# Performance work log

Measured on AMD Instinct MI355X. Metric: run time of the kernel, lower is better.

## Reference

```python
import jax, jax.numpy as jnp
import numpy as np

B, S, H, T, W = 8, 512, 768, 4, 10
NEG = -1e9

def _u(key, shape, k):
    return jax.random.uniform(key, shape, jnp.float32, -k, k)

def setup_inputs():
    key = jax.random.key(0)
    ks = jax.random.split(key, 20)
    kh = float(1.0 / np.sqrt(H)); kt = float(1.0 / np.sqrt(T))
    return dict(
        embeddings=jax.random.normal(ks[0], (B, S, H), jnp.float32),
        l1f_wih=_u(ks[1], (4 * H, H), kh), l1f_whh=_u(ks[2], (4 * H, H), kh), l1f_b=_u(ks[3], (4 * H,), kh),
        l1r_wih=_u(ks[4], (4 * H, H), kh), l1r_whh=_u(ks[5], (4 * H, H), kh), l1r_b=_u(ks[6], (4 * H,), kh),
        attn_w=_u(ks[7], (3 * H,), kh), attn_b=_u(ks[8], (1,), kh),
        l2f_wih=_u(ks[9], (4 * T, 2 * H), kt), l2f_whh=_u(ks[10], (4 * T, T), kt), l2f_b=_u(ks[11], (4 * T,), kt),
        l2r_wih=_u(ks[12], (4 * T, 2 * H), kt), l2r_whh=_u(ks[13], (4 * T, T), kt), l2r_b=_u(ks[14], (4 * T,), kt),
        crf_start=0.1 * jax.random.normal(ks[15], (T,), jnp.float32),
        crf_end=0.1 * jax.random.normal(ks[16], (T,), jnp.float32),
        crf_trans=0.1 * jax.random.normal(ks[17], (T, T), jnp.float32),
        window_size=W,
    )

def _lstm_dir(x, w_ih, w_hh, b):
    # x: [B,S,D] -> [B,S,Hh]; torch gate order i,f,g,o
    Hh = w_hh.shape[1]
    bs = x.shape[0]
    xs = (jnp.einsum('bsd,gd->bsg', x, w_ih) + b).transpose(1, 0, 2)  # [S,B,4Hh]
    def step(carry, xt):
        h, c = carry
        g = xt + h @ w_hh.T
        i, f, gg, o = jnp.split(g, 4, axis=-1)
        c = jax.nn.sigmoid(f) * c + jax.nn.sigmoid(i) * jnp.tanh(gg)
        h = jax.nn.sigmoid(o) * jnp.tanh(c)
        return (h, c), h
    init = (jnp.zeros((bs, Hh), x.dtype), jnp.zeros((bs, Hh), x.dtype))
    _, hs = jax.lax.scan(step, init, xs)
    return hs.transpose(1, 0, 2)

def _bilstm(x, pf, pr):
    hf = _lstm_dir(x, *pf)
    hr = _lstm_dir(x[:, ::-1], *pr)[:, ::-1]
    return jnp.concatenate([hf, hr], axis=-1)

def _win_attn(h, w, b, win):
    # h: [B,S,D]; similarity(hi,hj) = w1.hi + w2.hj + w3.(hi*hj) + b
    bs, s, d = h.shape
    w1, w2, w3 = w[:d], w[d:2 * d], w[2 * d:]
    offs = jnp.arange(-win, win + 1)                      # [K]
    idx = jnp.arange(s)[:, None] + offs[None, :]          # [S,K]
    valid = (idx >= 0) & (idx < s)
    idxc = jnp.clip(idx, 0, s - 1)
    hw = h[:, idxc]                                       # [B,S,K,D]
    scores = (h @ w1)[:, :, None] \
        + jnp.einsum('bskd,d->bsk', hw, w2) \
        + jnp.einsum('bsd,bskd->bsk', h * w3, hw) + b[0]
    scores = jnp.where(valid[None], scores, NEG)
    aw = jax.nn.softmax(scores, axis=-1)                  # [B,S,K]
    return jnp.einsum('bsk,bskd->bsd', aw, hw)

def _viterbi(em, start, end, trans):
    # em: [B,S,T] -> tags [B,S]
    score0 = start[None] + em[:, 0]
    ems = em.transpose(1, 0, 2)[1:]                       # [S-1,B,T]
    def step(score, e_t):
        nxt = score[:, :, None] + trans[None]             # [B,Tprev,T]
        best = jnp.max(nxt, axis=1) + e_t
        bp = jnp.argmax(nxt, axis=1)
        return best, bp
    final, bps = jax.lax.scan(step, score0, ems)          # bps [S-1,B,T]
    final = final + end[None]
    last = jnp.argmax(final, axis=-1)                     # [B]
    def back(tag, bp):
        prev = jnp.take_along_axis(bp, tag[:, None], axis=1)[:, 0]
        return prev, prev
    _, tags_rev = jax.lax.scan(back, last, bps[::-1])
    return jnp.concatenate([tags_rev[::-1], last[None]], axis=0).transpose(1, 0)

def reference(embeddings, l1f_wih, l1f_whh, l1f_b, l1r_wih, l1r_whh, l1r_b,
              attn_w, attn_b, l2f_wih, l2f_whh, l2f_b, l2r_wih, l2r_whh, l2r_b,
              crf_start, crf_end, crf_trans, window_size):
    h1 = _bilstm(embeddings, (l1f_wih, l1f_whh, l1f_b), (l1r_wih, l1r_whh, l1r_b))
    d = h1.shape[-1] // 2
    hs = h1[..., :d] + h1[..., d:]                        # sum of directions [B,S,H]
    att = _win_attn(hs, attn_w, attn_b, int(window_size))
    x2 = jnp.concatenate([hs, att], axis=-1)              # [B,S,2H]
    h2 = _bilstm(x2, (l2f_wih, l2f_whh, l2f_b), (l2r_wih, l2r_whh, l2r_b))
    d2 = h2.shape[-1] // 2
    em = h2[..., :d2] + h2[..., d2:]                      # CRF emissions [B,S,T]
    tags = _viterbi(em, crf_start, crf_end, crf_trans)
    return tags, em
```

## Files before the change

kernel.cpp:

```cpp
#include <hip/hip_runtime.h>
#include <math.h>

#define SEQ 512
#define BATCH 8
#define HID 768
#define G4 3072
#define CHUNK 128
#define NEGV (-1000000000.0f)

typedef float v4f __attribute__((ext_vector_type(4)));

__device__ __forceinline__ float sigm(float x) { return 1.0f / (1.0f + expf(-x)); }

__device__ __forceinline__ float wred(float x) {
#pragma unroll
  for (int off = 32; off > 0; off >>= 1) x += __shfl_xor(x, off, 64);
  return x;
}

__device__ __forceinline__ void load2_f4_sc(const float* p0, const float* p1,
                                            v4f& a, v4f& b) {
  asm volatile("global_load_dwordx4 %0, %2, off sc0 sc1\n\t"
               "global_load_dwordx4 %1, %3, off sc0 sc1\n\t"
               "s_waitcnt vmcnt(0)"
               : "=&v"(a), "=&v"(b) : "v"(p0), "v"(p1) : "memory");
}
__device__ __forceinline__ int load_i_sc(const int* p) {
  int r;
  asm volatile("global_load_dword %0, %1, off sc0 sc1\n\ts_waitcnt vmcnt(0)"
               : "=v"(r) : "v"(p) : "memory");
  return r;
}
__device__ __forceinline__ void store_f_sc(float* p, float v) {
  asm volatile("global_store_dword %0, %1, off sc0 sc1" :: "v"(p), "v"(v) : "memory");
}
__device__ __forceinline__ void store_i_sc(int* p, int v) {
  asm volatile("global_store_dword %0, %1, off sc0 sc1" :: "v"(p), "v"(v) : "memory");
}

template <int CTRL, int RMASK>
__device__ __forceinline__ float dpp_add(float x) {
  int y = __builtin_amdgcn_update_dpp(0, __float_as_int(x), CTRL, RMASK, 0xF, false);
  return x + __int_as_float(y);
}
__device__ __forceinline__ float reduce32(float x) {
  x = dpp_add<0x121, 0xF>(x);
  x = dpp_add<0x122, 0xF>(x);
  x = dpp_add<0x124, 0xF>(x);
  x = dpp_add<0x128, 0xF>(x);
  x = dpp_add<0x142, 0xA>(x);
  return x;
}

__global__ void k_init(float* __restrict__ hbuf, int* __restrict__ flags) {
  int i = blockIdx.x * blockDim.x + threadIdx.x;
  if (i < 2 * 2 * BATCH * HID) hbuf[i] = 0.0f;
  if (i < 4096) flags[i] = 0;
}

__global__ __launch_bounds__(256) void k_proj1(
    const float* __restrict__ emb,
    const float* __restrict__ w_f, const float* __restrict__ b_f,
    const float* __restrict__ w_r, const float* __restrict__ b_r,
    float* __restrict__ xs_f, float* __restrict__ xs_r, int chunk) {
  __shared__ float As[16][132];
  __shared__ float Bs[16][132];
  const int tid = threadIdx.x;
  const int bn0 = blockIdx.x * 128;
  const int bb  = blockIdx.y;
  const int dir = blockIdx.z;
  const float* W    = dir ? w_r : w_f;
  const float* bias = dir ? b_r : b_f;
  float* xs = dir ? xs_r : xs_f;

  float acc[8][8];
#pragma unroll
  for (int i = 0; i < 8; i++)
#pragma unroll
    for (int j = 0; j < 8; j++) acc[i][j] = 0.0f;

  const int mload = tid & 127;
  const int kq0   = tid >> 7;
  const int tglob = dir ? (SEQ - 1 - (chunk * CHUNK + mload)) : (chunk * CHUNK + mload);
  const float* arow = emb + (size_t)(bb * SEQ + tglob) * HID;
  const float* brow = W + (size_t)(bn0 + mload) * HID;
  const int tm = tid & 15, tn = tid >> 4;

  for (int kt = 0; kt < HID; kt += 16) {
#pragma unroll
    for (int rep = 0; rep < 2; rep++) {
      int kq = kq0 + rep * 2;
      float4 a = *(const float4*)(arow + kt + kq * 4);
      As[kq * 4 + 0][mload] = a.x; As[kq * 4 + 1][mload] = a.y;
      As[kq * 4 + 2][mload] = a.z; As[kq * 4 + 3][mload] = a.w;
      float4 b = *(const float4*)(brow + kt + kq * 4);
      Bs[kq * 4 + 0][mload] = b.x; Bs[kq * 4 + 1][mload] = b.y;
      Bs[kq * 4 + 2][mload] = b.z; Bs[kq * 4 + 3][mload] = b.w;
    }
    __syncthreads();
#pragma unroll
    for (int k = 0; k < 16; k++) {
      float4 a0 = *(const float4*)&As[k][tm * 8];
      float4 a1 = *(const float4*)&As[k][tm * 8 + 4];
      float4 b0 = *(const float4*)&Bs[k][tn * 8];
      float4 b1 = *(const float4*)&Bs[k][tn * 8 + 4];
      float av[8] = {a0.x, a0.y, a0.z, a0.w, a1.x, a1.y, a1.z, a1.w};
      float bv[8] = {b0.x, b0.y, b0.z, b0.w, b1.x, b1.y, b1.z, b1.w};
#pragma unroll
      for (int i = 0; i < 8; i++)
#pragma unroll
        for (int j = 0; j < 8; j++) acc[i][j] += av[i] * bv[j];
    }
    __syncthreads();
  }
#pragma unroll
  for (int i = 0; i < 8; i++) {
    int row = tm * 8 + i;
    size_t base = (size_t)(bb * CHUNK + row) * G4 + bn0 + tn * 8;
#pragma unroll
    for (int j = 0; j < 8; j++) xs[base + j] = acc[i][j] + bias[bn0 + tn * 8 + j];
  }
}

__global__ __launch_bounds__(384, 2) void k_rec1(
    const float* __restrict__ whh_f, const float* __restrict__ whh_r,
    const float* __restrict__ xs_f, const float* __restrict__ xs_r,
    float* __restrict__ hbuf, float* __restrict__ cbuf, int* __restrict__ flags,
    float* __restrict__ hf, float* __restrict__ hr, int t0, int init) {
  __shared__ float hlds[4 * HID];
  const int tid = threadIdx.x;
  const int bid = blockIdx.x;
  const int dir = bid >> 7;
  const int bh  = (bid >> 6) & 1;
  const int jb  = bid & 63;
  const int J0  = jb * 12;
  const int grp = dir * 2 + bh;
  const int g  = tid >> 5;
  const int kq = tid & 31;
  const int j  = J0 + g;

  const float* W  = dir ? whh_r : whh_f;
  const float* xs = dir ? xs_r  : xs_f;
  float* harr = dir ? hr : hf;

  float wreg[4][24];
#pragma unroll
  for (int gate = 0; gate < 4; gate++) {
#pragma unroll
    for (int q = 0; q < 6; q++) {
      *(v4f*)&wreg[gate][q * 4] =
          *(const v4f*)&W[(size_t)(gate * HID + j) * HID + q * 128 + kq * 4];
    }
  }

  float cc[4];
#pragma unroll
  for (int b = 0; b < 4; b++) cc[b] = 0.0f;
  if (!init && kq == 16) {
#pragma unroll
    for (int b = 0; b < 4; b++) cc[b] = cbuf[bid * 48 + g * 4 + b];
  }

  for (int stp = 0; stp < CHUNK; stp++) {
    const int s = t0 + stp;
    const int par = s & 1;

    float xsv[4][4];
    if (kq == 16) {
#pragma unroll
      for (int b = 0; b < 4; b++) {
        const size_t xbase = (size_t)((bh * 4 + b) * CHUNK + stp) * G4 + j;
#pragma unroll
        for (int gate = 0; gate < 4; gate++)
          xsv[b][gate] = xs[xbase + gate * HID];
      }
    }

    if (tid < 64) {
      const int* fp = flags + (grp * 64 + tid) * 16;
      while (load_i_sc(fp) < s) { __builtin_amdgcn_s_sleep(4); }
    }
    __syncthreads();

    {
      const float* src = hbuf + (size_t)((par * 2 + dir) * BATCH + bh * 4) * HID + tid * 8;
      v4f a, b4;
      load2_f4_sc(src, src + 4, a, b4);
      *(v4f*)&hlds[tid * 8]     = a;
      *(v4f*)&hlds[tid * 8 + 4] = b4;
    }
    __syncthreads();

    float acc[4][4];
#pragma unroll
    for (int gate = 0; gate < 4; gate++)
#pragma unroll
      for (int b = 0; b < 4; b++) acc[gate][b] = 0.0f;
#pragma unroll
    for (int b = 0; b < 4; b++) {
      float hk[24];
#pragma unroll
      for (int q = 0; q < 6; q++)
        *(v4f*)&hk[q * 4] = *(const v4f*)&hlds[b * HID + q * 128 + kq * 4];
#pragma unroll
      for (int gate = 0; gate < 4; gate++)
#pragma unroll
        for (int k = 0; k < 24; k++) acc[gate][b] += wreg[gate][k] * hk[k];
    }
#pragma unroll
    for (int gate = 0; gate < 4; gate++)
#pragma unroll
      for (int b = 0; b < 4; b++) acc[gate][b] = reduce32(acc[gate][b]);

    if (kq == 16) {
      const int t = dir ? (SEQ - 1 - s) : s;
#pragma unroll
      for (int b = 0; b < 4; b++) {
        const int bg = bh * 4 + b;
        float iv = acc[0][b] + xsv[b][0];
        float fv = acc[1][b] + xsv[b][1];
        float gv = acc[2][b] + xsv[b][2];
        float ov = acc[3][b] + xsv[b][3];
        cc[b] = sigm(fv) * cc[b] + sigm(iv) * tanhf(gv);
        float h = sigm(ov) * tanhf(cc[b]);
        store_f_sc(hbuf + (size_t)(((par ^ 1) * 2 + dir) * BATCH + bg) * HID + j, h);
        harr[(size_t)(bg * SEQ + t) * HID + j] = h;
      }
    }
    asm volatile("s_waitcnt vmcnt(0)" ::: "memory");
    __syncthreads();
    if (tid == 0) store_i_sc(flags + (grp * 64 + jb) * 16, s + 1);
  }
  if (kq == 16) {
#pragma unroll
    for (int b = 0; b < 4; b++) cbuf[bid * 48 + g * 4 + b] = cc[b];
  }
}

__global__ void k_sum(float* __restrict__ hf, const float* __restrict__ hr) {
  int i = blockIdx.x * 256 + threadIdx.x;
  float4 a = ((const float4*)hf)[i];
  float4 b = ((const float4*)hr)[i];
  a.x += b.x; a.y += b.y; a.z += b.z; a.w += b.w;
  ((float4*)hf)[i] = a;
}

__global__ __launch_bounds__(64) void k_attn(
    const float* __restrict__ hs, const float* __restrict__ attn_w,
    const float* __restrict__ attn_b, float* __restrict__ att) {
  const int l = threadIdx.x;
  const int s = blockIdx.x, b = blockIdx.y;
  const float* hrow = hs + (size_t)(b * SEQ + s) * HID;
  float v[12];
  float u1p = 0.0f;
#pragma unroll
  for (int jj = 0; jj < 12; jj++) {
    int d = l + 64 * jj;
    float x = hrow[d];
    u1p += x * attn_w[d];
    v[jj] = attn_w[HID + d] + x * attn_w[2 * HID + d];
  }
  float u1 = wred(u1p) + attn_b[0];
  float sc[21];
  for (int o = 0; o < 21; o++) {
    int s2 = s + o - 10;
    if (s2 >= 0 && s2 < SEQ) {
      const float* h2 = hs + (size_t)(b * SEQ + s2) * HID;
      float p = 0.0f;
#pragma unroll
      for (int jj = 0; jj < 12; jj++) p += h2[l + 64 * jj] * v[jj];
      sc[o] = wred(p) + u1;
    } else {
      sc[o] = NEGV;
    }
  }
  float m = sc[0];
#pragma unroll
  for (int o = 1; o < 21; o++) m = fmaxf(m, sc[o]);
  float sum = 0.0f;
#pragma unroll
  for (int o = 0; o < 21; o++) { sc[o] = expf(sc[o] - m); sum += sc[o]; }
  float inv = 1.0f / sum;
  float acc[12];
#pragma unroll
  for (int jj = 0; jj < 12; jj++) acc[jj] = 0.0f;
  for (int o = 0; o < 21; o++) {
    int s2 = s + o - 10;
    if (s2 < 0 || s2 >= SEQ) continue;
    float a = sc[o] * inv;
    const float* h2 = hs + (size_t)(b * SEQ + s2) * HID;
#pragma unroll
    for (int jj = 0; jj < 12; jj++) acc[jj] += a * h2[l + 64 * jj];
  }
  float* orow = att + (size_t)(b * SEQ + s) * HID;
#pragma unroll
  for (int jj = 0; jj < 12; jj++) orow[l + 64 * jj] = acc[jj];
}

__global__ __launch_bounds__(256) void k_proj2(
    const float* __restrict__ hs, const float* __restrict__ att,
    const float* __restrict__ w2f, const float* __restrict__ b2f,
    const float* __restrict__ w2r, const float* __restrict__ b2r,
    float* __restrict__ xs2) {
  __shared__ __align__(16) float x2[2 * HID];
  __shared__ float part[32][9];
  const int tid = threadIdx.x;
  const int s = blockIdx.x, b = blockIdx.y;
  size_t base = (size_t)(b * SEQ + s) * HID;
  for (int i = tid; i < 2 * HID; i += 256)
    x2[i] = (i < HID) ? hs[base + i] : att[base + i - HID];
  __syncthreads();
  const int gid = tid & 31, pp = tid >> 5;
  const int d = gid >> 4, g = gid & 15;
  const float4* w4 = (const float4*)((d ? w2r : w2f) + (size_t)g * (2 * HID));
  const float4* x4 = (const float4*)x2;
  float p = 0.0f;
  for (int e = pp * 48; e < pp * 48 + 48; e++) {
    float4 xv = x4[e];
    float4 wv = w4[e];
    p += xv.x * wv.x + xv.y * wv.y + xv.z * wv.z + xv.w * wv.w;
  }
  part[gid][pp] = p;
  __syncthreads();
  if (tid < 32) {
    float sumv = (d ? b2r : b2f)[g];
#pragma unroll
    for (int q = 0; q < 8; q++) sumv += part[gid][q];
    xs2[(size_t)((d * BATCH + b) * SEQ + s) * 16 + g] = sumv;
  }
}

__global__ __launch_bounds__(256) void k_rec2(
    const float* __restrict__ xs2,
    const float* __restrict__ whh_f, const float* __restrict__ whh_r,
    float* __restrict__ h2) {
  __shared__ float hsh[2 * BATCH * 4];
  __shared__ float gsh[2 * BATCH * 16];
  const int tid = threadIdx.x;
  const int d = tid >> 7, b = (tid >> 4) & 7, g = tid & 15;
  const float* whh = (d ? whh_r : whh_f) + g * 4;
  const float w0 = whh[0], w1 = whh[1], w2 = whh[2], w3 = whh[3];
  const int hb = d * BATCH + b;
  if (g < 4) hsh[hb * 4 + g] = 0.0f;
  float c = 0.0f;
  __syncthreads();
  const float* xrow = xs2 + (size_t)hb * SEQ * 16 + g;
  for (int st = 0; st < SEQ; st++) {
    int t = d ? (SEQ - 1 - st) : st;
    float gv = xrow[t * 16] + w0 * hsh[hb * 4 + 0] + w1 * hsh[hb * 4 + 1] +
               w2 * hsh[hb * 4 + 2] + w3 * hsh[hb * 4 + 3];
    gsh[hb * 16 + g] = gv;
    __syncthreads();
    if (g < 4) {
      float iv = gsh[hb * 16 + g];
      float fv = gsh[hb * 16 + 4 + g];
      float gq = gsh[hb * 16 + 8 + g];
      float ov = gsh[hb * 16 + 12 + g];
      c = sigm(fv) * c + sigm(iv) * tanhf(gq);
      float h = sigm(ov) * tanhf(c);
      hsh[hb * 4 + g] = h;
      h2[((size_t)hb * SEQ + t) * 4 + g] = h;
    }
    __syncthreads();
  }
}

__global__ void k_em(const float* __restrict__ h2, float* __restrict__ out) {
  int i = blockIdx.x * 256 + threadIdx.x;
  if (i < BATCH * SEQ * 4) out[BATCH * SEQ + i] = h2[i] + h2[BATCH * SEQ * 4 + i];
}

__global__ __launch_bounds__(32) void k_viterbi(
    float* __restrict__ out, const float* __restrict__ start,
    const float* __restrict__ endw, const float* __restrict__ trans) {
  __shared__ unsigned char bp[SEQ - 1][32];
  const int l = threadIdx.x;
  const int b = l >> 2, j = l & 3;
  const float* em = out + BATCH * SEQ;
  const float tr0 = trans[0 * 4 + j], tr1 = trans[1 * 4 + j];
  const float tr2 = trans[2 * 4 + j], tr3 = trans[3 * 4 + j];
  float score = start[j] + em[((size_t)b * SEQ + 0) * 4 + j];
  for (int t = 1; t < SEQ; t++) {
    float s0 = __shfl(score, b * 4 + 0, 64);
    float s1 = __shfl(score, b * 4 + 1, 64);
    float s2 = __shfl(score, b * 4 + 2, 64);
    float s3 = __shfl(score, b * 4 + 3, 64);
    float v0 = s0 + tr0, v1 = s1 + tr1, v2 = s2 + tr2, v3 = s3 + tr3;
    float best = v0; int arg = 0;
    if (v1 > best) { best = v1; arg = 1; }
    if (v2 > best) { best = v2; arg = 2; }
    if (v3 > best) { best = v3; arg = 3; }
    bp[t - 1][l] = (unsigned char)arg;
    score = best + em[((size_t)b * SEQ + t) * 4 + j];
  }
  score += endw[j];
  float f0 = __shfl(score, b * 4 + 0, 64);
  float f1 = __shfl(score, b * 4 + 1, 64);
  float f2 = __shfl(score, b * 4 + 2, 64);
  float f3 = __shfl(score, b * 4 + 3, 64);
  if (j == 0) {
    float bbv = f0; int last = 0;
    if (f1 > bbv) { bbv = f1; last = 1; }
    if (f2 > bbv) { bbv = f2; last = 2; }
    if (f3 > bbv) { bbv = f3; last = 3; }
    int tag = last;
    out[b * SEQ + (SEQ - 1)] = (float)tag;
    for (int t = SEQ - 2; t >= 0; t--) {
      tag = bp[t][b * 4 + tag];
      out[b * SEQ + t] = (float)tag;
    }
  }
}

extern "C" void kernel_launch(void* const* d_in, const int* in_sizes, int n_in,
                              void* d_out, int out_size, void* d_ws, size_t ws_size,
                              hipStream_t stream) {
  const float* emb      = (const float*)d_in[0];
  const float* l1f_wih  = (const float*)d_in[1];
  const float* l1f_whh  = (const float*)d_in[2];
  const float* l1f_b    = (const float*)d_in[3];
  const float* l1r_wih  = (const float*)d_in[4];
  const float* l1r_whh  = (const float*)d_in[5];
  const float* l1r_b    = (const float*)d_in[6];
  const float* attn_w   = (const float*)d_in[7];
  const float* attn_b   = (const float*)d_in[8];
  const float* l2f_wih  = (const float*)d_in[9];
  const float* l2f_whh  = (const float*)d_in[10];
  const float* l2f_b    = (const float*)d_in[11];
  const float* l2r_wih  = (const float*)d_in[12];
  const float* l2r_whh  = (const float*)d_in[13];
  const float* l2r_b    = (const float*)d_in[14];
  const float* crf_start= (const float*)d_in[15];
  const float* crf_end  = (const float*)d_in[16];
  const float* crf_trans= (const float*)d_in[17];

  float* ws = (float*)d_ws;
  const size_t NCH = (size_t)BATCH * CHUNK * G4;
  float* xs_f = ws;
  float* xs_r = xs_f + NCH;
  float* hf   = xs_r + NCH;
  float* hr   = hf + (size_t)BATCH * SEQ * HID;
  float* hbuf = hr + (size_t)BATCH * SEQ * HID;
  float* cbuf = hbuf + 2 * 2 * BATCH * HID;
  float* h2   = cbuf + 256 * 48;
  int*   flags= (int*)(h2 + 2 * BATCH * SEQ * 4);
  float* xs2  = xs_f;
  float* att  = xs_r;
  float* hs   = hf;

  k_init<<<dim3(96), dim3(256), 0, stream>>>(hbuf, flags);

  for (int c = 0; c < 4; c++) {
    k_proj1<<<dim3(24, 8, 2), dim3(256), 0, stream>>>(
        emb, l1f_wih, l1f_b, l1r_wih, l1r_b, xs_f, xs_r, c);
    k_rec1<<<dim3(256), dim3(384), 0, stream>>>(
        l1f_whh, l1r_whh, xs_f, xs_r, hbuf, cbuf, flags, hf, hr,
        c * CHUNK, c == 0 ? 1 : 0);
  }

  k_sum<<<dim3(3072), dim3(256), 0, stream>>>(hf, hr);
  k_attn<<<dim3(SEQ, BATCH), dim3(64), 0, stream>>>(hs, attn_w, attn_b, att);
  k_proj2<<<dim3(SEQ, BATCH), dim3(256), 0, stream>>>(
      hs, att, l2f_wih, l2f_b, l2r_wih, l2r_b, xs2);
  k_rec2<<<dim3(1), dim3(256), 0, stream>>>(xs2, l2f_whh, l2r_whh, h2);
  k_em<<<dim3(64), dim3(256), 0, stream>>>(h2, (float*)d_out);
  k_viterbi<<<dim3(1), dim3(32), 0, stream>>>((float*)d_out, crf_start, crf_end, crf_trans);
}
```

Measured before the change: 3.892 ms.

## Spread LSTM cell update across threads, fuse direction sum, shuffle-based layer-2 recurrence

In the layer-1 recurrent kernel, gate partial sums now pass through shared memory so 48 threads each update one (unit, batch) cell instead of 12 lanes each doing four batches. The trailing block barrier before the flag store is dropped and the spin-wait sleep is shortened. The separate direction-sum kernel is removed, with attention and projection summing hf+hr on the fly. The layer-2 recurrence is rewritten to use one wavefront per (direction, batch) with shuffles and prefetched inputs, so there are no block-wide barriers per step. Removing the barrier before the flag publish relies on waitcnt ordering in the first wave only, which may be a correctness risk for stores made by other waves.

Measured after the change: 4.049 ms. 4.0% more time.

```diff
diff --git a/kernel.cpp b/kernel.cpp
--- a/kernel.cpp
+++ b/kernel.cpp
@@ -128,6 +128,7 @@
     float* __restrict__ hbuf, float* __restrict__ cbuf, int* __restrict__ flags,
     float* __restrict__ hf, float* __restrict__ hr, int t0, int init) {
   __shared__ float hlds[4 * HID];
+  __shared__ float psl[192];
   const int tid = threadIdx.x;
   const int bid = blockIdx.x;
   const int dir = bid >> 7;
@@ -138,6 +139,8 @@
   const int g  = tid >> 5;
   const int kq = tid & 31;
   const int j  = J0 + g;
+  const int ej = tid >> 2;
+  const int eb = tid & 3;
 
   const float* W  = dir ? whh_r : whh_f;
   const float* xs = dir ? xs_r  : xs_f;
@@ -153,32 +156,24 @@
     }
   }
 
-  float cc[4];
-#pragma unroll
-  for (int b = 0; b < 4; b++) cc[b] = 0.0f;
-  if (!init && kq == 16) {
-#pragma unroll
-    for (int b = 0; b < 4; b++) cc[b] = cbuf[bid * 48 + g * 4 + b];
-  }
+  float cc = 0.0f;
+  if (!init && tid < 48) cc = cbuf[bid * 48 + tid];
 
   for (int stp = 0; stp < CHUNK; stp++) {
     const int s = t0 + stp;
     const int par = s & 1;
 
-    float xsv[4][4];
-    if (kq == 16) {
-#pragma unroll
-      for (int b = 0; b < 4; b++) {
-        const size_t xbase = (size_t)((bh * 4 + b) * CHUNK + stp) * G4 + j;
-#pragma unroll
-        for (int gate = 0; gate < 4; gate++)
-          xsv[b][gate] = xs[xbase + gate * HID];
-      }
-    }
-
+    float exs0 = 0.f, exs1 = 0.f, exs2 = 0.f, exs3 = 0.f;
+    if (tid < 48) {
+      const size_t xbase = (size_t)((bh * 4 + eb) * CHUNK + stp) * G4 + J0 + ej;
+      exs0 = xs[xbase + 0 * HID];
+      exs1 = xs[xbase + 1 * HID];
+      exs2 = xs[xbase + 2 * HID];
+      exs3 = xs[xbase + 3 * HID];
+    }
     if (tid < 64) {
       const int* fp = flags + (grp * 64 + tid) * 16;
-      while (load_i_sc(fp) < s) { __builtin_amdgcn_s_sleep(4); }
+      while (load_i_sc(fp) < s) { __builtin_amdgcn_s_sleep(1); }
     }
     __syncthreads();
 
@@ -191,72 +186,71 @@
     }
     __syncthreads();
 
+    float hk[4][24];
+#pragma unroll
+    for (int b = 0; b < 4; b++)
+#pragma unroll
+      for (int q = 0; q < 6; q++)
+        *(v4f*)&hk[b][q * 4] = *(const v4f*)&hlds[b * HID + q * 128 + kq * 4];
+
     float acc[4][4];
 #pragma unroll
     for (int gate = 0; gate < 4; gate++)
 #pragma unroll
       for (int b = 0; b < 4; b++) acc[gate][b] = 0.0f;
 #pragma unroll
-    for (int b = 0; b < 4; b++) {
-      float hk[24];
-#pragma unroll
-      for (int q = 0; q < 6; q++)
-        *(v4f*)&hk[q * 4] = *(const v4f*)&hlds[b * HID + q * 128 + kq * 4];
+    for (int b = 0; b < 4; b++)
 #pragma unroll
       for (int gate = 0; gate < 4; gate++)
 #pragma unroll
-        for (int k = 0; k < 24; k++) acc[gate][b] += wreg[gate][k] * hk[k];
-    }
+        for (int k = 0; k < 24; k++) acc[gate][b] += wreg[gate][k] * hk[b][k];
+
 #pragma unroll
     for (int gate = 0; gate < 4; gate++)
 #pragma unroll
       for (int b = 0; b < 4; b++) acc[gate][b] = reduce32(acc[gate][b]);
 
     if (kq == 16) {
+#pragma unroll
+      for (int gate = 0; gate < 4; gate++)
+#pragma unroll
+        for (int b = 0; b < 4; b++) psl[(g * 4 + gate) * 4 + b] = acc[gate][b];
+    }
+    __syncthreads();
+
+    if (tid < 48) {
+      float iv = psl[(ej * 4 + 0) * 4 + eb] + exs0;
+      float fv = psl[(ej * 4 + 1) * 4 + eb] + exs1;
+      float gv = psl[(ej * 4 + 2) * 4 + eb] + exs2;
+      float ov = psl[(ej * 4 + 3) * 4 + eb] + exs3;
+      cc = sigm(fv) * cc + sigm(iv) * tanhf(gv);
+      float h = sigm(ov) * tanhf(cc);
       const int t = dir ? (SEQ - 1 - s) : s;
-#pragma unroll
-      for (int b = 0; b < 4; b++) {
-        const int bg = bh * 4 + b;
-        float iv = acc[0][b] + xsv[b][0];
-        float fv = acc[1][b] + xsv[b][1];
-        float gv = acc[2][b] + xsv[b][2];
-        float ov = acc[3][b] + xsv[b][3];
-        cc[b] = sigm(fv) * cc[b] + sigm(iv) * tanhf(gv);
-        float h = sigm(ov) * tanhf(cc[b]);
-        store_f_sc(hbuf + (size_t)(((par ^ 1) * 2 + dir) * BATCH + bg) * HID + j, h);
-        harr[(size_t)(bg * SEQ + t) * HID + j] = h;
-      }
-    }
-    asm volatile("s_waitcnt vmcnt(0)" ::: "memory");
-    __syncthreads();
-    if (tid == 0) store_i_sc(flags + (grp * 64 + jb) * 16, s + 1);
-  }
-  if (kq == 16) {
-#pragma unroll
-    for (int b = 0; b < 4; b++) cbuf[bid * 48 + g * 4 + b] = cc[b];
-  }
-}
-
-__global__ void k_sum(float* __restrict__ hf, const float* __restrict__ hr) {
-  int i = blockIdx.x * 256 + threadIdx.x;
-  float4 a = ((const float4*)hf)[i];
-  float4 b = ((const float4*)hr)[i];
-  a.x += b.x; a.y += b.y; a.z += b.z; a.w += b.w;
-  ((float4*)hf)[i] = a;
+      const int bg = bh * 4 + eb;
+      store_f_sc(hbuf + (size_t)(((par ^ 1) * 2 + dir) * BATCH + bg) * HID + J0 + ej, h);
+      harr[(size_t)(bg * SEQ + t) * HID + J0 + ej] = h;
+    }
+    if (tid < 64) {
+      asm volatile("s_waitcnt vmcnt(0)" ::: "memory");
+      if (tid == 0) store_i_sc(flags + (grp * 64 + jb) * 16, s + 1);
+    }
+  }
+  if (tid < 48) cbuf[bid * 48 + tid] = cc;
 }
 
 __global__ __launch_bounds__(64) void k_attn(
-    const float* __restrict__ hs, const float* __restrict__ attn_w,
-    const float* __restrict__ attn_b, float* __restrict__ att) {
+    const float* __restrict__ hf, const float* __restrict__ hr,
+    const float* __restrict__ attn_w, const float* __restrict__ attn_b,
+    float* __restrict__ att) {
   const int l = threadIdx.x;
   const int s = blockIdx.x, b = blockIdx.y;
-  const float* hrow = hs + (size_t)(b * SEQ + s) * HID;
+  const size_t rbase = (size_t)(b * SEQ + s) * HID;
   float v[12];
   float u1p = 0.0f;
 #pragma unroll
   for (int jj = 0; jj < 12; jj++) {
     int d = l + 64 * jj;
-    float x = hrow[d];
+    float x = hf[rbase + d] + hr[rbase + d];
     u1p += x * attn_w[d];
     v[jj] = attn_w[HID + d] + x * attn_w[2 * HID + d];
   }
@@ -265,10 +259,13 @@
   for (int o = 0; o < 21; o++) {
     int s2 = s + o - 10;
     if (s2 >= 0 && s2 < SEQ) {
-      const float* h2 = hs + (size_t)(b * SEQ + s2) * HID;
+      const size_t b2 = (size_t)(b * SEQ + s2) * HID;
       float p = 0.0f;
 #pragma unroll
-      for (int jj = 0; jj < 12; jj++) p += h2[l + 64 * jj] * v[jj];
+      for (int jj = 0; jj < 12; jj++) {
+        int d = l + 64 * jj;
+        p += (hf[b2 + d] + hr[b2 + d]) * v[jj];
+      }
       sc[o] = wred(p) + u1;
     } else {
       sc[o] = NEGV;
@@ -288,17 +285,21 @@
     int s2 = s + o - 10;
     if (s2 < 0 || s2 >= SEQ) continue;
     float a = sc[o] * inv;
-    const float* h2 = hs + (size_t)(b * SEQ + s2) * HID;
-#pragma unroll
-    for (int jj = 0; jj < 12; jj++) acc[jj] += a * h2[l + 64 * jj];
-  }
-  float* orow = att + (size_t)(b * SEQ + s) * HID;
+    const size_t b2 = (size_t)(b * SEQ + s2) * HID;
+#pragma unroll
+    for (int jj = 0; jj < 12; jj++) {
+      int d = l + 64 * jj;
+      acc[jj] += a * (hf[b2 + d] + hr[b2 + d]);
+    }
+  }
+  float* orow = att + rbase;
 #pragma unroll
   for (int jj = 0; jj < 12; jj++) orow[l + 64 * jj] = acc[jj];
 }
 
 __global__ __launch_bounds__(256) void k_proj2(
-    const float* __restrict__ hs, const float* __restrict__ att,
+    const float* __restrict__ hf, const float* __restrict__ hr,
+    const float* __restrict__ att,
     const float* __restrict__ w2f, const float* __restrict__ b2f,
     const float* __restrict__ w2r, const float* __restrict__ b2r,
     float* __restrict__ xs2) {
@@ -308,7 +309,7 @@
   const int s = blockIdx.x, b = blockIdx.y;
   size_t base = (size_t)(b * SEQ + s) * HID;
   for (int i = tid; i < 2 * HID; i += 256)
-    x2[i] = (i < HID) ? hs[base + i] : att[base + i - HID];
+    x2[i] = (i < HID) ? (hf[base + i] + hr[base + i]) : att[base + i - HID];
   __syncthreads();
   const int gid = tid & 31, pp = tid >> 5;
   const int d = gid >> 4, g = gid & 15;
@@ -330,38 +331,41 @@
   }
 }
 
-__global__ __launch_bounds__(256) void k_rec2(
+__global__ __launch_bounds__(1024) void k_rec2(
     const float* __restrict__ xs2,
     const float* __restrict__ whh_f, const float* __restrict__ whh_r,
     float* __restrict__ h2) {
-  __shared__ float hsh[2 * BATCH * 4];
-  __shared__ float gsh[2 * BATCH * 16];
   const int tid = threadIdx.x;
-  const int d = tid >> 7, b = (tid >> 4) & 7, g = tid & 15;
-  const float* whh = (d ? whh_r : whh_f) + g * 4;
-  const float w0 = whh[0], w1 = whh[1], w2 = whh[2], w3 = whh[3];
+  const int w = tid >> 6;
+  const int l = tid & 63;
+  const int d = w >> 3, b = w & 7;
   const int hb = d * BATCH + b;
-  if (g < 4) hsh[hb * 4 + g] = 0.0f;
-  float c = 0.0f;
-  __syncthreads();
-  const float* xrow = xs2 + (size_t)hb * SEQ * 16 + g;
-  for (int st = 0; st < SEQ; st++) {
-    int t = d ? (SEQ - 1 - st) : st;
-    float gv = xrow[t * 16] + w0 * hsh[hb * 4 + 0] + w1 * hsh[hb * 4 + 1] +
-               w2 * hsh[hb * 4 + 2] + w3 * hsh[hb * 4 + 3];
-    gsh[hb * 16 + g] = gv;
-    __syncthreads();
-    if (g < 4) {
-      float iv = gsh[hb * 16 + g];
-      float fv = gsh[hb * 16 + 4 + g];
-      float gq = gsh[hb * 16 + 8 + g];
-      float ov = gsh[hb * 16 + 12 + g];
-      c = sigm(fv) * c + sigm(iv) * tanhf(gq);
-      float h = sigm(ov) * tanhf(c);
-      hsh[hb * 4 + g] = h;
-      h2[((size_t)hb * SEQ + t) * 4 + g] = h;
-    }
-    __syncthreads();
+  if (l < 16) {
+    const float* whh = (d ? whh_r : whh_f) + l * 4;
+    const float w0 = whh[0], w1 = whh[1], w2 = whh[2], w3 = whh[3];
+    const float* xrow = xs2 + (size_t)hb * SEQ * 16 + l;
+    float c = 0.0f, hval = 0.0f;
+    float xcur = xrow[(d ? (SEQ - 1) : 0) * 16];
+    for (int st = 0; st < SEQ; st++) {
+      const int t = d ? (SEQ - 1 - st) : st;
+      const int tn = d ? (SEQ - 2 - st) : (st + 1);
+      float xnext = (st + 1 < SEQ) ? xrow[tn * 16] : 0.0f;
+      float h0 = __shfl(hval, 0, 64);
+      float h1 = __shfl(hval, 1, 64);
+      float h2v = __shfl(hval, 2, 64);
+      float h3 = __shfl(hval, 3, 64);
+      float gv = xcur + w0 * h0 + w1 * h1 + w2 * h2v + w3 * h3;
+      float iv = __shfl(gv, (l & 3) + 0, 64);
+      float fv = __shfl(gv, (l & 3) + 4, 64);
+      float gg = __shfl(gv, (l & 3) + 8, 64);
+      float ov = __shfl(gv, (l & 3) + 12, 64);
+      if (l < 4) {
+        c = sigm(fv) * c + sigm(iv) * tanhf(gg);
+        hval = sigm(ov) * tanhf(c);
+        h2[((size_t)hb * SEQ + t) * 4 + l] = hval;
+      }
+      xcur = xnext;
+    }
   }
 }
 
@@ -446,7 +450,6 @@
   int*   flags= (int*)(h2 + 2 * BATCH * SEQ * 4);
   float* xs2  = xs_f;
   float* att  = xs_r;
-  float* hs   = hf;
 
   k_init<<<dim3(96), dim3(256), 0, stream>>>(hbuf, flags);
 
@@ -458,11 +461,10 @@
         c * CHUNK, c == 0 ? 1 : 0);
   }
 
-  k_sum<<<dim3(3072), dim3(256), 0, stream>>>(hf, hr);
-  k_attn<<<dim3(SEQ, BATCH), dim3(64), 0, stream>>>(hs, attn_w, attn_b, att);
+  k_attn<<<dim3(SEQ, BATCH), dim3(64), 0, stream>>>(hf, hr, attn_w, attn_b, att);
   k_proj2<<<dim3(SEQ, BATCH), dim3(256), 0, stream>>>(
-      hs, att, l2f_wih, l2f_b, l2r_wih, l2r_b, xs2);
-  k_rec2<<<dim3(1), dim3(256), 0, stream>>>(xs2, l2f_whh, l2r_whh, h2);
+      hf, hr, att, l2f_wih, l2f_b, l2r_wih, l2r_b, xs2);
+  k_rec2<<<dim3(1), dim3(1024), 0, stream>>>(xs2, l2f_whh, l2r_whh, h2);
   k_em<<<dim3(64), dim3(256), 0, stream>>>(h2, (float*)d_out);
   k_viterbi<<<dim3(1), dim3(32), 0, stream>>>((float*)d_out, crf_start, crf_end, crf_trans);
 }
```
